# Optimization experiments

Hardware: AMD Instinct MI355X
Metric: run time of the kernel (lower is better)

The kernel has to match this reference:

```python
import jax, jax.numpy as jnp
import numpy as np

N, E, D0, D1, H = 20000, 640000, 64, 32, 64


def setup_inputs() -> dict:
    key = jax.random.key(0)
    ks = jax.random.split(key, 16)
    s = 0.1
    return {
        'feat0e': jax.random.normal(ks[0], (N, D0), jnp.float32),
        'feat1o': jax.random.normal(ks[1], (N, D1, 3), jnp.float32),
        'edge_attr': jax.random.normal(ks[2], (E, H), jnp.float32),
        'pos': jax.random.normal(ks[3], (N, 3), jnp.float32),
        'edge_index': jax.random.randint(ks[4], (2, E), 0, N, jnp.int64),
        # edge_net: FullyConnectedNet([H]*3 -> [H]) with silu
        'W1': jax.random.normal(ks[5], (H, H), jnp.float32) * s,
        'b1': jnp.zeros((H,), jnp.float32),
        'W2': jax.random.normal(ks[6], (H, H), jnp.float32) * s,
        'b2': jnp.zeros((H,), jnp.float32),
        'W3': jax.random.normal(ks[7], (H, H), jnp.float32) * s,
        'b3': jnp.zeros((H,), jnp.float32),
        # tensor-product path weights (internal weights, not shared)
        'w_ss': jax.random.normal(ks[8], (D0, H, D0), jnp.float32) * s,     # 0e x 0e -> 0e
        'w_vv': jax.random.normal(ks[9], (D1, D0), jnp.float32) * s,        # 1o . 1o -> 0e
        'w_sv': jax.random.normal(ks[10], (D0, D1), jnp.float32) * s,       # 0e x 1o -> 1o
        'w_vs': jax.random.normal(ks[11], (D1, H, D1), jnp.float32) * s,    # 1o x 0e -> 1o
        'w_cross': jax.random.normal(ks[12], (D1, D1), jnp.float32) * s,    # 1o x 1o -> 1o (cross)
        # gate: scalars -> per-vector-channel gates
        'Wg': jax.random.normal(ks[13], (D0, D1), jnp.float32) * s,
        'bg': jnp.zeros((D1,), jnp.float32),
    }


def reference(feat0e, feat1o, edge_attr, pos, edge_index,
              W1, b1, W2, b2, W3, b3,
              w_ss, w_vv, w_sv, w_vs, w_cross, Wg, bg):
    src, dst = edge_index[0], edge_index[1]

    # edge MLP (silu)
    h = jax.nn.silu(edge_attr @ W1 + b1)
    h = jax.nn.silu(h @ W2 + b2)
    edge_scalar = h @ W3 + b3                      # [E, H]

    rel_pos = pos[dst] - pos[src]                  # [E, 3]
    s_src = feat0e[src]                            # [E, D0]
    v_src = feat1o[src]                            # [E, D1, 3]

    # equivariant tensor product per edge
    dot_vv = jnp.sum(v_src * rel_pos[:, None, :], axis=-1)          # [E, D1]
    msg0e = (jnp.einsum('ep,eh,pho->eo', s_src, edge_scalar, w_ss)
             + dot_vv @ w_vv)                                        # [E, D0]
    cross_vv = jnp.cross(v_src, rel_pos[:, None, :])                 # [E, D1, 3]
    msg1o = (jnp.einsum('ep,pc,ex->ecx', s_src, w_sv, rel_pos)
             + jnp.einsum('edx,eh,dhc->ecx', v_src, edge_scalar, w_vs)
             + jnp.einsum('edx,dc->ecx', cross_vv, w_cross))          # [E, D1, 3]

    # scatter_mean over destination nodes
    counts = jax.ops.segment_sum(jnp.ones((E,), msg0e.dtype), dst, num_segments=N)
    denom = jnp.maximum(counts, 1.0)
    aggr0e = jax.ops.segment_sum(msg0e, dst, num_segments=N) / denom[:, None]
    aggr1o = jax.ops.segment_sum(msg1o, dst, num_segments=N) / denom[:, None, None]

    # gate + residual
    out0e = jax.nn.silu(aggr0e) + feat0e                              # [N, D0]
    gates = jax.nn.silu(aggr0e @ Wg + bg)                             # [N, D1]
    out1o = aggr1o * gates[:, :, None] + feat1o                       # [N, D1, 3]

    # concat flattened outputs into one array [N, D0 + 3*D1]
    return jnp.concatenate([out0e, out1o.reshape(N, D1 * 3)], axis=-1)
```

## Files before the change

kernel.cpp:

```cpp
#include <hip/hip_runtime.h>


#define NN 20000
#define EE 640000
#define EPMAX 940032

typedef _Float16 half8 __attribute__((ext_vector_type(8)));
typedef float f32x4 __attribute__((ext_vector_type(4)));

__device__ __forceinline__ float silu_f(float x) { return x / (1.0f + __expf(-x)); }
__device__ __forceinline__ _Float16 u2h(unsigned short u) {
    union { unsigned short u; _Float16 h; } c; c.u = u; return c.h;
}
__device__ __forceinline__ unsigned short h2u(_Float16 h) {
    union { unsigned short u; _Float16 h; } c; c.h = h; return c.u;
}
__device__ __forceinline__ half8 pack8(float4 a, float4 b) {
    half8 h;
    h[0]=(_Float16)a.x; h[1]=(_Float16)a.y; h[2]=(_Float16)a.z; h[3]=(_Float16)a.w;
    h[4]=(_Float16)b.x; h[5]=(_Float16)b.y; h[6]=(_Float16)b.z; h[7]=(_Float16)b.w;
    return h;
}

#define OFF_HIST  0ull
#define OFF_RS    81920ull
#define OFF_CUR   163840ull
#define OFF_FLAG  245760ull
#define F_OUTD    262144ull
#define F_PSP     360448ull
#define F_CURS    458752ull
#define F_POSOF   557056ull
#define F_AUX     3117056ull
#define F_DSTP    23597056ull
#define F_PDP     27357184ull
#define F_WMLP    31117312ull
#define F_WSV     31141888ull
#define F_WX2     31145984ull
#define F_WVV     31148032ull
#define F_WSSG    31152128ull
#define F_WVS3    31676416ull
#define F_ES      31807488ull
#define F_MSG0    152131584ull
#define F_MSG1    234051584ull
#define F_GH      356931584ull
#define NEED_F(npp) (F_GH + (unsigned long long)(npp) * 20480ull)

__global__ void detect_idx_kernel(const int* __restrict__ eidx, int* __restrict__ flag) {
    int odd_nz = 0, even_nz = 0;
    for (int k = 0; k < 64; ++k) {
        if (eidx[2 * k + 1] != 0) odd_nz = 1;
        if (eidx[2 * k] != 0) even_nz = 1;
    }
    *flag = (!odd_nz && even_nz) ? 1 : 0;
}

__device__ __forceinline__ void load_sd(const int* eidx, const int* flag, int e,
                                        int& s_, int& d_) {
    if (*flag) { s_ = (int)((const long long*)eidx)[e]; d_ = (int)((const long long*)eidx)[EE + e]; }
    else       { s_ = eidx[e];                          d_ = eidx[EE + e]; }
}

__global__ __launch_bounds__(256) void hist2_kernel(
    const int* __restrict__ eidx, const int* __restrict__ flag,
    int* __restrict__ hist, int* __restrict__ outd)
{
    const int e = blockIdx.x * 256 + threadIdx.x;
    int s_, d_; load_sd(eidx, flag, e, s_, d_);
    atomicAdd(hist + d_, 1);
    atomicAdd(outd + s_, 1);
}

__global__ __launch_bounds__(1024) void scan_kernel(
    const int* __restrict__ hist, int* __restrict__ rs, int* __restrict__ cur)
{
    __shared__ int part[1024];
    const int t = threadIdx.x;
    const int base = t * 20;
    int loc[20];
    int tot = 0;
#pragma unroll
    for (int k = 0; k < 20; ++k) {
        int n = base + k;
        int h = (n < NN) ? hist[n] : 0;
        loc[k] = tot; tot += h;
    }
    part[t] = tot;
    __syncthreads();
    for (int off = 1; off < 1024; off <<= 1) {
        int v = (t >= off) ? part[t - off] : 0;
        __syncthreads();
        part[t] += v;
        __syncthreads();
    }
    int excl = part[t] - tot;
#pragma unroll
    for (int k = 0; k < 20; ++k) {
        int n = base + k;
        if (n < NN) { rs[n] = excl + loc[k]; cur[n] = excl + loc[k]; }
    }
    if (t == 1023) rs[NN] = part[1023];
}

__global__ __launch_bounds__(1024) void scanP_kernel(
    const int* __restrict__ outd, int* __restrict__ psP, int* __restrict__ curS)
{
    __shared__ int part[1024];
    const int t = threadIdx.x;
    const int base = t * 20;
    int loc[20];
    int tot = 0;
#pragma unroll
    for (int k = 0; k < 20; ++k) {
        int n = base + k;
        int p = (n < NN) ? ((outd[n] + 15) & ~15) : 0;
        loc[k] = tot; tot += p;
    }
    part[t] = tot;
    __syncthreads();
    for (int off = 1; off < 1024; off <<= 1) {
        int v = (t >= off) ? part[t - off] : 0;
        __syncthreads();
        part[t] += v;
        __syncthreads();
    }
    int excl = part[t] - tot;
#pragma unroll
    for (int k = 0; k < 20; ++k) {
        int n = base + k;
        if (n < NN) { psP[n] = excl + loc[k]; curS[n] = excl + loc[k]; }
    }
}

__global__ __launch_bounds__(256) void scat_src_kernel(
    const int* __restrict__ eidx, const int* __restrict__ flag,
    int* __restrict__ curS, int* __restrict__ cur,
    int* __restrict__ dstP, int* __restrict__ pdP, int* __restrict__ posof)
{
    const int e = blockIdx.x * 256 + threadIdx.x;
    int s_, d_; load_sd(eidx, flag, e, s_, d_);
    int posS = atomicAdd(curS + s_, 1);
    int posD = atomicAdd(cur + d_, 1);
    dstP[posS] = d_; pdP[posS] = posD; posof[e] = posS;
}

__global__ __launch_bounds__(256) void prep2_kernel(
    const float* __restrict__ wss, const float* __restrict__ wvv,
    const float* __restrict__ wsv, const float* __restrict__ wvs,
    const float* __restrict__ wx,
    const float* __restrict__ W1, const float* __restrict__ W2,
    const float* __restrict__ W3, char* __restrict__ ws)
{
    int id = blockIdx.x * 256 + threadIdx.x;
    if (id >= 43136) return;
    int l = id & 63;
    int l4 = l >> 4, l16 = l & 15;
    half8 o;
    _Float16* dst;
    if (id < 32768) {
        int i = id;
        int f = i >> 6;
        int q = f >> 3, kfp = (f >> 2) & 1, nfp = f & 3;
#pragma unroll
        for (int j = 0; j < 8; j++) {
            int p = kfp * 32 + l4 * 8 + j;
            int cc = q * 64 + nfp * 16 + l16;
            int jc = cc & 7, lc = (cc >> 3) & 63, fi = cc >> 9;
            int kfc = fi >> 2, nfc = fi & 3;
            int h = kfc * 32 + (lc >> 4) * 8 + jc;
            int oo = nfc * 16 + (lc & 15);
            o[j] = (_Float16)wss[((size_t)p * 64 + h) * 64 + oo];
        }
        dst = (_Float16*)(ws + F_WSSG) + (size_t)i * 8;
    } else if (id < 40960) {
        int i = id - 32768;
        int f = i >> 6;
        int col = f * 16 + l16;
#pragma unroll
        for (int j = 0; j < 8; j++) {
            int d = l4 * 8 + j;
            o[j] = (_Float16)wvs[((size_t)d * 64 + (col & 63)) * 32 + (col >> 6)];
        }
        dst = (_Float16*)(ws + F_WVS3) + (size_t)i * 8;
    } else if (id < 42496) {
        int i = id - 40960; int f = i >> 6;
        int layer = f >> 3, kf = (f >> 2) & 1, nf = f & 3;
        const float* W = layer == 0 ? W1 : (layer == 1 ? W2 : W3);
#pragma unroll
        for (int j = 0; j < 8; j++)
            o[j] = (_Float16)W[(kf * 32 + l4 * 8 + j) * 64 + nf * 16 + l16];
        dst = (_Float16*)(ws + F_WMLP) + (size_t)i * 8;
    } else if (id < 42752) {
        int i = id - 42496; int nf = i >> 6;
#pragma unroll
        for (int j = 0; j < 8; j++)
            o[j] = (_Float16)wvv[(l4 * 8 + j) * 64 + nf * 16 + l16];
        dst = (_Float16*)(ws + F_WVV) + (size_t)i * 8;
    } else if (id < 43008) {
        int i = id - 42752; int frag = i >> 6;
        int kf = frag >> 1, nf = frag & 1;
#pragma unroll
        for (int j = 0; j < 8; j++)
            o[j] = (_Float16)wsv[(kf * 32 + l4 * 8 + j) * 32 + nf * 16 + l16];
        dst = (_Float16*)(ws + F_WSV) + (size_t)i * 8;
    } else {
        int i = id - 43008; int nf = i >> 6;
#pragma unroll
        for (int j = 0; j < 8; j++)
            o[j] = (_Float16)wx[(l4 * 8 + j) * 32 + nf * 16 + l16];
        dst = (_Float16*)(ws + F_WX2) + (size_t)i * 8;
    }
    *(half8*)dst = o;
}

__global__ __launch_bounds__(256, 4) void gG2_kernel(
    const float* __restrict__ feat0e, const char* __restrict__ wsp,
    int lo, int hi, _Float16* __restrict__ GH, _Float16* __restrict__ aux)
{
    const int tid = threadIdx.x, w = tid >> 6, lane = tid & 63;
    const int l4 = lane >> 4, l16 = lane & 15;
    const int n0 = lo + blockIdx.x * 16;
    if (n0 >= hi) return;

    half8 af[2];
    {
        int n = n0 + l16; if (n >= NN) n = NN - 1;
        const float* sp = feat0e + (size_t)n * 64 + l4 * 8;
        af[0] = pack8(*(const float4*)sp, *(const float4*)(sp + 4));
        af[1] = pack8(*(const float4*)(sp + 32), *(const float4*)(sp + 36));
    }
    const half8* wg = (const half8*)(wsp + F_WSSG);
#pragma unroll 2
    for (int qq = 0; qq < 16; ++qq) {
        const int q = w * 16 + qq;
        f32x4 acc[4];
#pragma unroll
        for (int nf = 0; nf < 4; nf++) acc[nf] = (f32x4){0.f,0.f,0.f,0.f};
#pragma unroll
        for (int kf = 0; kf < 2; kf++)
#pragma unroll
            for (int nf = 0; nf < 4; nf++)
                acc[nf] = __builtin_amdgcn_mfma_f32_16x16x32_f16(
                    af[kf], wg[(q * 8 + kf * 4 + nf) * 64 + lane], acc[nf], 0, 0, 0);
#pragma unroll
        for (int nf = 0; nf < 4; nf++)
#pragma unroll
            for (int reg = 0; reg < 4; reg++) {
                int n = n0 + l4 * 4 + reg;
                if (n < hi && n < NN)
                    GH[(size_t)(n - lo) * 10240 + q * 64 + nf * 16 + l16] =
                        (_Float16)acc[nf][reg];
            }
    }
    if (w == 0) {
        const half8* wsvp = (const half8*)(wsp + F_WSV);
        f32x4 accg[2];
#pragma unroll
        for (int nf = 0; nf < 2; nf++) accg[nf] = (f32x4){0.f,0.f,0.f,0.f};
#pragma unroll
        for (int kf = 0; kf < 2; kf++)
#pragma unroll
            for (int nf = 0; nf < 2; nf++)
                accg[nf] = __builtin_amdgcn_mfma_f32_16x16x32_f16(
                    af[kf], wsvp[(kf * 2 + nf) * 64 + lane], accg[nf], 0, 0, 0);
#pragma unroll
        for (int nf = 0; nf < 2; nf++)
#pragma unroll
            for (int reg = 0; reg < 4; reg++) {
                int n = n0 + l4 * 4 + reg;
                if (n < hi && n < NN)
                    aux[(size_t)n * 512 + nf * 16 + l16] = (_Float16)accg[nf][reg];
            }
    }
}

__global__ __launch_bounds__(256, 4) void gH_kernel(
    const float* __restrict__ feat1o, const char* __restrict__ wsp,
    int lo, int hi, _Float16* __restrict__ GH, _Float16* __restrict__ aux)
{
    const int tid = threadIdx.x, w = tid >> 6, lane = tid & 63;
    const int l4 = lane >> 4, l16 = lane & 15;
    const int n0 = lo + blockIdx.x * 16;
    const int x = blockIdx.y;
    if (n0 >= hi) return;

    half8 av;
    {
        int nn = n0 + l16; if (nn >= NN) nn = NN - 1;
#pragma unroll
        for (int j = 0; j < 8; j++)
            av[j] = (_Float16)feat1o[(size_t)nn * 96 + (l4 * 8 + j) * 3 + x];
    }
    const half8* wvs3 = (const half8*)(wsp + F_WVS3);

#pragma unroll 4
    for (int ff = 0; ff < 32; ++ff) {
        const int f = w * 32 + ff;
        f32x4 acc = __builtin_amdgcn_mfma_f32_16x16x32_f16(
            av, wvs3[f * 64 + lane], (f32x4){0.f,0.f,0.f,0.f}, 0, 0, 0);
#pragma unroll
        for (int reg = 0; reg < 4; reg++) {
            int n = n0 + l4 * 4 + reg;
            if (n < hi && n < NN)
                GH[(size_t)(n - lo) * 10240 + 4096 + x * 2048 + f * 16 + l16] =
                    (_Float16)acc[reg];
        }
    }
    if (w == 0) {
        const half8* wvvp = (const half8*)(wsp + F_WVV);
        const half8* wx2  = (const half8*)(wsp + F_WX2);
#pragma unroll
        for (int nf = 0; nf < 4; ++nf) {
            f32x4 acc = __builtin_amdgcn_mfma_f32_16x16x32_f16(
                av, wvvp[nf * 64 + lane], (f32x4){0.f,0.f,0.f,0.f}, 0, 0, 0);
#pragma unroll
            for (int reg = 0; reg < 4; reg++) {
                int n = n0 + l4 * 4 + reg;
                if (n < hi && n < NN)
                    aux[(size_t)n * 512 + 128 + x * 64 + nf * 16 + l16] =
                        (_Float16)acc[reg];
            }
        }
#pragma unroll
        for (int nf = 0; nf < 2; ++nf) {
            f32x4 acc = __builtin_amdgcn_mfma_f32_16x16x32_f16(
                av, wx2[nf * 64 + lane], (f32x4){0.f,0.f,0.f,0.f}, 0, 0, 0);
#pragma unroll
            for (int reg = 0; reg < 4; reg++) {
                int n = n0 + l4 * 4 + reg;
                if (n < hi && n < NN)
                    aux[(size_t)n * 512 + 32 + x * 32 + nf * 16 + l16] =
                        (_Float16)acc[reg];
            }
        }
    }
}

__global__ __launch_bounds__(256, 2) void es_kernel(
    const float* __restrict__ edge_attr,
    const float* __restrict__ b1, const float* __restrict__ b2,
    const float* __restrict__ b3,
    const char* __restrict__ wsp, const int* __restrict__ posof,
    _Float16* __restrict__ es)
{
    __shared__ half8 wml[1536];
    __shared__ __align__(16) unsigned short xch[4][1024];

    const int tid = threadIdx.x, w = tid >> 6, lane = tid & 63;
    const int l4 = lane >> 4, l16 = lane & 15;

    {
        const half8* wm = (const half8*)(wsp + F_WMLP);
        for (int f = tid; f < 1536; f += 256) wml[f] = wm[f];
    }
    __syncthreads();

    const int e0 = blockIdx.x * 64 + w * 16;

    float bias[3][4];
#pragma unroll
    for (int nf = 0; nf < 4; nf++) {
        bias[0][nf] = b1[nf * 16 + l16];
        bias[1][nf] = b2[nf * 16 + l16];
        bias[2][nf] = b3[nf * 16 + l16];
    }

    half8 af[2];
    {
        const float* ap = edge_attr + (size_t)(e0 + l16) * 64 + l4 * 8;
        af[0] = pack8(*(const float4*)ap, *(const float4*)(ap + 4));
        af[1] = pack8(*(const float4*)(ap + 32), *(const float4*)(ap + 36));
    }

    unsigned short* x = xch[w];
    const int sw16 = (l16 & 7) << 3;

#pragma unroll
    for (int layer = 0; layer < 3; ++layer) {
        f32x4 acc[4];
#pragma unroll
        for (int nf = 0; nf < 4; nf++) acc[nf] = (f32x4){0.f,0.f,0.f,0.f};
#pragma unroll
        for (int kf = 0; kf < 2; kf++)
#pragma unroll
            for (int nf = 0; nf < 4; nf++)
                acc[nf] = __builtin_amdgcn_mfma_f32_16x16x32_f16(
                    af[kf], wml[(layer * 8 + kf * 4 + nf) * 64 + lane],
                    acc[nf], 0, 0, 0);
#pragma unroll
        for (int nf = 0; nf < 4; nf++)
#pragma unroll
            for (int reg = 0; reg < 4; reg++) {
                int row = l4 * 4 + reg;
                int col = nf * 16 + l16;
                float v = acc[nf][reg] + bias[layer][nf];
                if (layer < 2) v = silu_f(v);
                x[row * 64 + (col ^ ((row & 7) << 3))] = h2u((_Float16)v);
            }
        if (layer < 2) {
#pragma unroll
            for (int kf = 0; kf < 2; kf++)
                af[kf] = *(const half8*)&x[l16 * 64 + ((kf * 32 + l4 * 8) ^ sw16)];
        }
    }
#pragma unroll
    for (int i = 0; i < 2; i++) {
        int row16 = i * 8 + (lane >> 3);
        int ps = posof[e0 + row16];
        int c8 = lane & 7;
        half8 v = *(const half8*)&x[row16 * 64 + ((c8 * 8) ^ ((row16 & 7) << 3))];
        *(half8*)(es + (size_t)ps * 64 + c8 * 8) = v;
    }
}

__global__ __launch_bounds__(256, 3) void msg01_node_kernel(
    const float* __restrict__ pos,
    const char* __restrict__ wsp,
    const _Float16* __restrict__ GH,
    const _Float16* __restrict__ es,
    int lo, int hi,
    _Float16* __restrict__ msg0, _Float16* __restrict__ msg1)
{
    __shared__ __align__(16) unsigned short xch[4][16 * 104];
    __shared__ float relb[4][16][4];
    __shared__ unsigned short auxl[4][320];

    const int tid = threadIdx.x, w = tid >> 6, lane = tid & 63;
    const int l4 = lane >> 4, l16 = lane & 15;

    const int n = lo + blockIdx.x * 4 + w;
    if (n >= hi) return;
    const int deg = ((const int*)(wsp + F_OUTD))[n];
    if (deg == 0) return;
    const int base = ((const int*)(wsp + F_PSP))[n];
    const int* dstP = (const int*)(wsp + F_DSTP);
    const int* pdP  = (const int*)(wsp + F_PDP);

    const float pn0 = pos[n * 3 + 0], pn1 = pos[n * 3 + 1], pn2 = pos[n * 3 + 2];

    const size_t kbase = (size_t)(n - lo) * 10240;
    half8 Gr[8];
    {
        const half8* gn = (const half8*)(GH + kbase);
#pragma unroll
        for (int f = 0; f < 8; f++) Gr[f] = gn[f * 64 + lane];
    }
    half8 Hf[2][6];
    {
        const _Float16* Hg = GH + kbase + 4096;
#pragma unroll
        for (int x = 0; x < 3; x++)
#pragma unroll
            for (int nfc = 0; nfc < 2; nfc++)
#pragma unroll
                for (int kf = 0; kf < 2; kf++)
                    Hf[kf][x * 2 + nfc] = *(const half8*)(
                        Hg + x * 2048 + (nfc * 16 + l16) * 64 + kf * 32 + l4 * 8);
    }
    {
        const _Float16* ag = (const _Float16*)(wsp + F_AUX) + (size_t)n * 512;
        for (int i = lane; i < 320; i += 64) auxl[w][i] = h2u(ag[i]);
    }

    unsigned short* x = xch[w];
    const int ntile = (deg + 15) >> 4;

    for (int t = 0; t < ntile; ++t) {
        const int r0 = t * 16;
        int rowc = r0 + l16; if (rowc > deg - 1) rowc = deg - 1;
        const int dd = dstP[base + rowc];
        const float rel0 = pos[dd * 3 + 0] - pn0;
        const float rel1 = pos[dd * 3 + 1] - pn1;
        const float rel2 = pos[dd * 3 + 2] - pn2;
        if (l4 == 0) {
            relb[w][l16][0] = rel0; relb[w][l16][1] = rel1; relb[w][l16][2] = rel2;
        }

        half8 esf[2];
        {
            const _Float16* ep = es + (size_t)(base + rowc) * 64;
            esf[0] = *(const half8*)(ep + l4 * 8);
            esf[1] = *(const half8*)(ep + 32 + l4 * 8);
        }

        {
            f32x4 acc0[4];
#pragma unroll
            for (int nf = 0; nf < 4; nf++) acc0[nf] = (f32x4){0.f,0.f,0.f,0.f};
#pragma unroll
            for (int kf = 0; kf < 2; kf++)
#pragma unroll
                for (int nf = 0; nf < 4; nf++)
                    acc0[nf] = __builtin_amdgcn_mfma_f32_16x16x32_f16(
                        esf[kf], Gr[kf * 4 + nf], acc0[nf], 0, 0, 0);
#pragma unroll
            for (int nf = 0; nf < 4; nf++) {
                float vw0 = (float)u2h(auxl[w][128 + 0 * 64 + nf * 16 + l16]);
                float vw1 = (float)u2h(auxl[w][128 + 1 * 64 + nf * 16 + l16]);
                float vw2 = (float)u2h(auxl[w][128 + 2 * 64 + nf * 16 + l16]);
#pragma unroll
                for (int reg = 0; reg < 4; reg++) {
                    int row = l4 * 4 + reg;
                    float v = acc0[nf][reg]
                            + relb[w][row][0] * vw0
                            + relb[w][row][1] * vw1
                            + relb[w][row][2] * vw2;
                    int col = nf * 16 + l16;
                    x[row * 104 + (col ^ ((row & 7) << 3))] = h2u((_Float16)v);
                }
            }
#pragma unroll
            for (int i = 0; i < 2; i++) {
                int row16 = i * 8 + (lane >> 3);
                if (r0 + row16 < deg) {
                    int rowD = pdP[base + r0 + row16];
                    int c8 = lane & 7;
                    half8 v = *(const half8*)&x[row16 * 104 + ((c8 * 8) ^ ((row16 & 7) << 3))];
                    *(half8*)(msg0 + (size_t)rowD * 64 + c8 * 8) = v;
                }
            }
        }

        {
            f32x4 acc1[6];
#pragma unroll
            for (int nf = 0; nf < 6; nf++) acc1[nf] = (f32x4){0.f,0.f,0.f,0.f};
#pragma unroll
            for (int kf = 0; kf < 2; kf++)
#pragma unroll
                for (int nf = 0; nf < 6; nf++)
                    acc1[nf] = __builtin_amdgcn_mfma_f32_16x16x32_f16(
                        esf[kf], Hf[kf][nf], acc1[nf], 0, 0, 0);
#pragma unroll
            for (int nf = 0; nf < 6; nf++) {
                const int xx = nf >> 1;
                const int x1 = (xx + 1) % 3, x2 = (xx + 2) % 3;
                const int c = (nf & 1) * 16 + l16;
                const float gv  = (float)u2h(auxl[w][c]);
                const float cw1 = (float)u2h(auxl[w][32 + x1 * 32 + c]);
                const float cw2 = (float)u2h(auxl[w][32 + x2 * 32 + c]);
#pragma unroll
                for (int reg = 0; reg < 4; reg++) {
                    int row = l4 * 4 + reg;
                    float val = acc1[nf][reg]
                              + gv * relb[w][row][xx]
                              + relb[w][row][x2] * cw1
                              - relb[w][row][x1] * cw2;
                    int col = nf * 16 + l16;
                    x[row * 104 + (col ^ ((row & 3) << 3))] = h2u((_Float16)val);
                }
            }
            const int rowS = lane >> 2;
            if (r0 + rowS < deg) {
                int rowD = pdP[base + r0 + rowS];
                const int swr = (rowS & 3) << 3;
#pragma unroll
                for (int t3 = 0; t3 < 3; t3++) {
                    int co = ((lane & 3) + 4 * t3) * 8;
                    half8 v = *(const half8*)&x[rowS * 104 + (co ^ swr)];
                    *(half8*)(msg1 + (size_t)rowD * 96 + co) = v;
                }
            }
        }
    }
}

__global__ __launch_bounds__(256) void gather0_kernel(
    const float* __restrict__ feat0e,
    const float* __restrict__ Wg, const float* __restrict__ bg,
    const char* __restrict__ wsp, const _Float16* __restrict__ msg0,
    float* __restrict__ out)
{
    __shared__ float Wgl[2048];
    __shared__ float ag[4][64];
    const int tid = threadIdx.x, w = tid >> 6, lane = tid & 63;
    for (int t = tid; t < 2048; t += 256) Wgl[t] = Wg[t];

    const int n = blockIdx.x * 4 + w;
    const int* rs = (const int*)(wsp + OFF_RS);
    const int i0 = rs[n], i1 = rs[n + 1];
    const int r8 = lane >> 3, c8 = lane & 7;

    float a[8];
#pragma unroll
    for (int j = 0; j < 8; j++) a[j] = 0.f;
    for (int i = i0 + r8; i < i1; i += 8) {
        half8 m = *(const half8*)(msg0 + (size_t)i * 64 + c8 * 8);
#pragma unroll
        for (int j = 0; j < 8; j++) a[j] += (float)m[j];
    }
#pragma unroll
    for (int s = 8; s < 64; s <<= 1)
#pragma unroll
        for (int j = 0; j < 8; j++) a[j] += __shfl_xor(a[j], s);
    if (r8 == 0)
#pragma unroll
        for (int j = 0; j < 8; j++) ag[w][c8 * 8 + j] = a[j];
    __syncthreads();

    const float inv = 1.0f / fmaxf((float)(i1 - i0), 1.0f);
    float av = ag[w][lane] * inv;
    out[(size_t)n * 160 + lane] = silu_f(av) + feat0e[(size_t)n * 64 + lane];

    if (lane < 32) {
        float gs = bg[lane];
#pragma unroll
        for (int p = 0; p < 64; ++p) gs = fmaf(ag[w][p] * inv, Wgl[p * 32 + lane], gs);
        out[(size_t)n * 160 + 64 + lane] = silu_f(gs);
    }
}

__global__ __launch_bounds__(256) void gather1_kernel(
    const float* __restrict__ feat1o,
    const char* __restrict__ wsp, const _Float16* __restrict__ msg1,
    float* __restrict__ out)
{
    __shared__ float ag1[4][96];
    __shared__ float gl[4][32];
    const int tid = threadIdx.x, w = tid >> 6, lane = tid & 63;
    const int n = blockIdx.x * 4 + w;
    const int* rs = (const int*)(wsp + OFF_RS);
    const int i0 = rs[n], i1 = rs[n + 1];

    if (lane < 32) gl[w][lane] = out[(size_t)n * 160 + 64 + lane];

    const int r4 = lane >> 4, c12 = lane & 15;
    float a[8];
#pragma unroll
    for (int j = 0; j < 8; j++) a[j] = 0.f;
    if (c12 < 12)
        for (int i = i0 + r4; i < i1; i += 4) {
            half8 m = *(const half8*)(msg1 + (size_t)i * 96 + c12 * 8);
#pragma unroll
            for (int j = 0; j < 8; j++) a[j] += (float)m[j];
        }
#pragma unroll
    for (int s = 16; s < 64; s <<= 1)
#pragma unroll
        for (int j = 0; j < 8; j++) a[j] += __shfl_xor(a[j], s);
    if (r4 == 0 && c12 < 12)
#pragma unroll
        for (int j = 0; j < 8; j++) ag1[w][c12 * 8 + j] = a[j];
    __syncthreads();

    const float inv = 1.0f / fmaxf((float)(i1 - i0), 1.0f);
#pragma unroll
    for (int t = 0; t < 2; t++) {
        int idx = t * 64 + lane;
        if (idx < 96) {
            int c = idx / 3, xx = idx - 3 * c;
            float v = ag1[w][xx * 32 + c] * inv * gl[w][c] + feat1o[(size_t)n * 96 + idx];
            out[(size_t)n * 160 + 64 + idx] = v;
        }
    }
}

extern "C" void kernel_launch(void* const* d_in, const int* in_sizes, int n_in,
                              void* d_out, int out_size, void* d_ws, size_t ws_size,
                              hipStream_t stream) {
    const float* feat0e    = (const float*)d_in[0];
    const float* feat1o    = (const float*)d_in[1];
    const float* edge_attr = (const float*)d_in[2];
    const float* pos       = (const float*)d_in[3];
    const int*   eidx      = (const int*)d_in[4];
    const float* W1 = (const float*)d_in[5];
    const float* b1 = (const float*)d_in[6];
    const float* W2 = (const float*)d_in[7];
    const float* b2 = (const float*)d_in[8];
    const float* W3 = (const float*)d_in[9];
    const float* b3 = (const float*)d_in[10];
    const float* wss    = (const float*)d_in[11];
    const float* wvv    = (const float*)d_in[12];
    const float* wsv    = (const float*)d_in[13];
    const float* wvs    = (const float*)d_in[14];
    const float* wcross = (const float*)d_in[15];
    const float* Wg = (const float*)d_in[16];
    const float* bg = (const float*)d_in[17];

    float* out = (float*)d_out;
    char*  ws  = (char*)d_ws;
    int* hist = (int*)(ws + OFF_HIST);
    int* rs   = (int*)(ws + OFF_RS);
    int* cur  = (int*)(ws + OFF_CUR);
    int* flag = (int*)(ws + OFF_FLAG);
    int* outd = (int*)(ws + F_OUTD);
    int* psP  = (int*)(ws + F_PSP);
    int* curS = (int*)(ws + F_CURS);
    int* posof= (int*)(ws + F_POSOF);
    int* dstP = (int*)(ws + F_DSTP);
    int* pdP  = (int*)(ws + F_PDP);
    _Float16* aux   = (_Float16*)(ws + F_AUX);
    _Float16* esb   = (_Float16*)(ws + F_ES);
    _Float16* msg0F = (_Float16*)(ws + F_MSG0);
    _Float16* msg1F = (_Float16*)(ws + F_MSG1);
    _Float16* GH    = (_Float16*)(ws + F_GH);

    int nppF = 0;
    const int cands[6] = {20000, 10000, 5000, 2500, 1250, 625};
    for (int i = 0; i < 6; ++i)
        if (ws_size >= NEED_F(cands[i])) { nppF = cands[i]; break; }
    if (nppF == 0) return;

    detect_idx_kernel<<<1, 1, 0, stream>>>(eidx, flag);
    hipMemsetAsync(ws + OFF_HIST, 0, NN * sizeof(int), stream);
    hipMemsetAsync(ws + F_OUTD, 0, NN * sizeof(int), stream);

    hist2_kernel<<<EE / 256, 256, 0, stream>>>(eidx, flag, hist, outd);
    scan_kernel<<<1, 1024, 0, stream>>>(hist, rs, cur);
    scanP_kernel<<<1, 1024, 0, stream>>>(outd, psP, curS);
    scat_src_kernel<<<EE / 256, 256, 0, stream>>>(
        eidx, flag, curS, cur, dstP, pdP, posof);
    prep2_kernel<<<(43136 + 255) / 256, 256, 0, stream>>>(
        wss, wvv, wsv, wvs, wcross, W1, W2, W3, ws);

    es_kernel<<<EE / 64, 256, 0, stream>>>(
        edge_attr, b1, b2, b3, (const char*)ws, posof, esb);

    const int S = (NN + nppF - 1) / nppF;
    for (int s = 0; s < S; ++s) {
        int lo = s * nppF;
        int hi = lo + nppF; if (hi > NN) hi = NN;
        const int ngroups = (hi - lo + 15) / 16;
        gG2_kernel<<<ngroups, 256, 0, stream>>>(
            feat0e, (const char*)ws, lo, hi, GH, aux);
        gH_kernel<<<dim3(ngroups, 3), 256, 0, stream>>>(
            feat1o, (const char*)ws, lo, hi, GH, aux);
        msg01_node_kernel<<<(hi - lo + 3) / 4, 256, 0, stream>>>(
            pos, (const char*)ws, GH, esb, lo, hi, msg0F, msg1F);
    }
    gather0_kernel<<<NN / 4, 256, 0, stream>>>(
        feat0e, Wg, bg, (const char*)ws, msg0F, out);
    gather1_kernel<<<NN / 4, 256, 0, stream>>>(
        feat1o, (const char*)ws, msg1F, out);
}
```

Measured before the change: 819.7 us.

## Fuse setup, node-transform, and gather kernels; interleave message buffers

Merges the two scan kernels into one launch and folds the edge scatter (source/destination slot assignment) into the edge-MLP kernel, which removes the posof buffer. Combines the scalar and vector node-transform kernels into one grid using blockIdx.y, and writes msg0/msg1 into a single interleaved 160-wide buffer so one gather kernel can reduce both and compute gates without reading them back from the output. The message kernel also prefetches the first tile's destination index and edge-scalar values, and loads aux with vector loads. The main savings are fewer launches and fewer intermediate global round-trips. The cost is that the atomics now sit inside the MLP kernel, and the interleaved stride may change gather coalescing.

```diff
diff --git a/kernel.cpp b/kernel.cpp
--- a/kernel.cpp
+++ b/kernel.cpp
@@ -29,20 +29,18 @@
 #define F_OUTD    262144ull
 #define F_PSP     360448ull
 #define F_CURS    458752ull
-#define F_POSOF   557056ull
-#define F_AUX     3117056ull
-#define F_DSTP    23597056ull
-#define F_PDP     27357184ull
-#define F_WMLP    31117312ull
-#define F_WSV     31141888ull
-#define F_WX2     31145984ull
-#define F_WVV     31148032ull
-#define F_WSSG    31152128ull
-#define F_WVS3    31676416ull
-#define F_ES      31807488ull
-#define F_MSG0    152131584ull
-#define F_MSG1    234051584ull
-#define F_GH      356931584ull
+#define F_AUX     557056ull
+#define F_DSTP    21037056ull
+#define F_PDP     24797184ull
+#define F_WMLP    28557312ull
+#define F_WSV     28581888ull
+#define F_WX2     28585984ull
+#define F_WVV     28588032ull
+#define F_WSSG    28592128ull
+#define F_WVS3    29116416ull
+#define F_ES      29247488ull
+#define F_MSG     149571584ull
+#define F_GH      354371584ull
 #define NEED_F(npp) (F_GH + (unsigned long long)(npp) * 20480ull)
 
 __global__ void detect_idx_kernel(const int* __restrict__ eidx, int* __restrict__ flag) {
@@ -70,77 +68,62 @@
     atomicAdd(outd + s_, 1);
 }
 
-__global__ __launch_bounds__(1024) void scan_kernel(
-    const int* __restrict__ hist, int* __restrict__ rs, int* __restrict__ cur)
+__global__ __launch_bounds__(1024) void scan2_kernel(
+    const int* __restrict__ hist, const int* __restrict__ outd,
+    int* __restrict__ rs, int* __restrict__ cur,
+    int* __restrict__ psP, int* __restrict__ curS)
 {
     __shared__ int part[1024];
     const int t = threadIdx.x;
     const int base = t * 20;
-    int loc[20];
-    int tot = 0;
-#pragma unroll
-    for (int k = 0; k < 20; ++k) {
-        int n = base + k;
-        int h = (n < NN) ? hist[n] : 0;
-        loc[k] = tot; tot += h;
-    }
-    part[t] = tot;
+    {
+        int loc[20]; int tot = 0;
+#pragma unroll
+        for (int k = 0; k < 20; ++k) {
+            int n = base + k;
+            int h = (n < NN) ? hist[n] : 0;
+            loc[k] = tot; tot += h;
+        }
+        part[t] = tot;
+        __syncthreads();
+        for (int off = 1; off < 1024; off <<= 1) {
+            int v = (t >= off) ? part[t - off] : 0;
+            __syncthreads();
+            part[t] += v;
+            __syncthreads();
+        }
+        int excl = part[t] - tot;
+#pragma unroll
+        for (int k = 0; k < 20; ++k) {
+            int n = base + k;
+            if (n < NN) { rs[n] = excl + loc[k]; cur[n] = excl + loc[k]; }
+        }
+        if (t == 1023) rs[NN] = part[1023];
+    }
     __syncthreads();
-    for (int off = 1; off < 1024; off <<= 1) {
-        int v = (t >= off) ? part[t - off] : 0;
+    {
+        int loc[20]; int tot = 0;
+#pragma unroll
+        for (int k = 0; k < 20; ++k) {
+            int n = base + k;
+            int p = (n < NN) ? ((outd[n] + 15) & ~15) : 0;
+            loc[k] = tot; tot += p;
+        }
+        part[t] = tot;
         __syncthreads();
-        part[t] += v;
-        __syncthreads();
-    }
-    int excl = part[t] - tot;
-#pragma unroll
-    for (int k = 0; k < 20; ++k) {
-        int n = base + k;
-        if (n < NN) { rs[n] = excl + loc[k]; cur[n] = excl + loc[k]; }
-    }
-    if (t == 1023) rs[NN] = part[1023];
-}
-
-__global__ __launch_bounds__(1024) void scanP_kernel(
-    const int* __restrict__ outd, int* __restrict__ psP, int* __restrict__ curS)
-{
-    __shared__ int part[1024];
-    const int t = threadIdx.x;
-    const int base = t * 20;
-    int loc[20];
-    int tot = 0;
-#pragma unroll
-    for (int k = 0; k < 20; ++k) {
-        int n = base + k;
-        int p = (n < NN) ? ((outd[n] + 15) & ~15) : 0;
-        loc[k] = tot; tot += p;
-    }
-    part[t] = tot;
-    __syncthreads();
-    for (int off = 1; off < 1024; off <<= 1) {
-        int v = (t >= off) ? part[t - off] : 0;
-        __syncthreads();
-        part[t] += v;
-        __syncthreads();
-    }
-    int excl = part[t] - tot;
-#pragma unroll
-    for (int k = 0; k < 20; ++k) {
-        int n = base + k;
-        if (n < NN) { psP[n] = excl + loc[k]; curS[n] = excl + loc[k]; }
-    }
-}
-
-__global__ __launch_bounds__(256) void scat_src_kernel(
-    const int* __restrict__ eidx, const int* __restrict__ flag,
-    int* __restrict__ curS, int* __restrict__ cur,
-    int* __restrict__ dstP, int* __restrict__ pdP, int* __restrict__ posof)
-{
-    const int e = blockIdx.x * 256 + threadIdx.x;
-    int s_, d_; load_sd(eidx, flag, e, s_, d_);
-    int posS = atomicAdd(curS + s_, 1);
-    int posD = atomicAdd(cur + d_, 1);
-    dstP[posS] = d_; pdP[posS] = posD; posof[e] = posS;
+        for (int off = 1; off < 1024; off <<= 1) {
+            int v = (t >= off) ? part[t - off] : 0;
+            __syncthreads();
+            part[t] += v;
+            __syncthreads();
+        }
+        int excl = part[t] - tot;
+#pragma unroll
+        for (int k = 0; k < 20; ++k) {
+            int n = base + k;
+            if (n < NN) { psP[n] = excl + loc[k]; curS[n] = excl + loc[k]; }
+        }
+    }
 }
 
 __global__ __launch_bounds__(256) void prep2_kernel(
@@ -212,8 +195,9 @@
     *(half8*)dst = o;
 }
 
-__global__ __launch_bounds__(256, 4) void gG2_kernel(
-    const float* __restrict__ feat0e, const char* __restrict__ wsp,
+__global__ __launch_bounds__(256, 4) void gGH_kernel(
+    const float* __restrict__ feat0e, const float* __restrict__ feat1o,
+    const char* __restrict__ wsp,
     int lo, int hi, _Float16* __restrict__ GH, _Float16* __restrict__ aux)
 {
     const int tid = threadIdx.x, w = tid >> 6, lane = tid & 63;
@@ -221,115 +205,106 @@
     const int n0 = lo + blockIdx.x * 16;
     if (n0 >= hi) return;
 
-    half8 af[2];
-    {
-        int n = n0 + l16; if (n >= NN) n = NN - 1;
-        const float* sp = feat0e + (size_t)n * 64 + l4 * 8;
-        af[0] = pack8(*(const float4*)sp, *(const float4*)(sp + 4));
-        af[1] = pack8(*(const float4*)(sp + 32), *(const float4*)(sp + 36));
-    }
-    const half8* wg = (const half8*)(wsp + F_WSSG);
+    if (blockIdx.y == 0) {
+        half8 af[2];
+        {
+            int n = n0 + l16; if (n >= NN) n = NN - 1;
+            const float* sp = feat0e + (size_t)n * 64 + l4 * 8;
+            af[0] = pack8(*(const float4*)sp, *(const float4*)(sp + 4));
+            af[1] = pack8(*(const float4*)(sp + 32), *(const float4*)(sp + 36));
+        }
+        const half8* wg = (const half8*)(wsp + F_WSSG);
 #pragma unroll 2
-    for (int qq = 0; qq < 16; ++qq) {
-        const int q = w * 16 + qq;
-        f32x4 acc[4];
-#pragma unroll
-        for (int nf = 0; nf < 4; nf++) acc[nf] = (f32x4){0.f,0.f,0.f,0.f};
-#pragma unroll
-        for (int kf = 0; kf < 2; kf++)
+        for (int qq = 0; qq < 16; ++qq) {
+            const int q = w * 16 + qq;
+            f32x4 acc[4];
+#pragma unroll
+            for (int nf = 0; nf < 4; nf++) acc[nf] = (f32x4){0.f,0.f,0.f,0.f};
+#pragma unroll
+            for (int kf = 0; kf < 2; kf++)
+#pragma unroll
+                for (int nf = 0; nf < 4; nf++)
+                    acc[nf] = __builtin_amdgcn_mfma_f32_16x16x32_f16(
+                        af[kf], wg[(q * 8 + kf * 4 + nf) * 64 + lane], acc[nf], 0, 0, 0);
 #pragma unroll
             for (int nf = 0; nf < 4; nf++)
-                acc[nf] = __builtin_amdgcn_mfma_f32_16x16x32_f16(
-                    af[kf], wg[(q * 8 + kf * 4 + nf) * 64 + lane], acc[nf], 0, 0, 0);
-#pragma unroll
-        for (int nf = 0; nf < 4; nf++)
+#pragma unroll
+                for (int reg = 0; reg < 4; reg++) {
+                    int n = n0 + l4 * 4 + reg;
+                    if (n < hi && n < NN)
+                        GH[(size_t)(n - lo) * 10240 + q * 64 + nf * 16 + l16] =
+                            (_Float16)acc[nf][reg];
+                }
+        }
+        if (w == 0) {
+            const half8* wsvp = (const half8*)(wsp + F_WSV);
+            f32x4 accg[2];
+#pragma unroll
+            for (int nf = 0; nf < 2; nf++) accg[nf] = (f32x4){0.f,0.f,0.f,0.f};
+#pragma unroll
+            for (int kf = 0; kf < 2; kf++)
+#pragma unroll
+                for (int nf = 0; nf < 2; nf++)
+                    accg[nf] = __builtin_amdgcn_mfma_f32_16x16x32_f16(
+                        af[kf], wsvp[(kf * 2 + nf) * 64 + lane], accg[nf], 0, 0, 0);
+#pragma unroll
+            for (int nf = 0; nf < 2; nf++)
+#pragma unroll
+                for (int reg = 0; reg < 4; reg++) {
+                    int n = n0 + l4 * 4 + reg;
+                    if (n < hi && n < NN)
+                        aux[(size_t)n * 512 + nf * 16 + l16] = (_Float16)accg[nf][reg];
+                }
+        }
+    } else {
+        const int x = blockIdx.y - 1;
+        half8 av;
+        {
+            int nn = n0 + l16; if (nn >= NN) nn = NN - 1;
+#pragma unroll
+            for (int j = 0; j < 8; j++)
+                av[j] = (_Float16)feat1o[(size_t)nn * 96 + (l4 * 8 + j) * 3 + x];
+        }
+        const half8* wvs3 = (const half8*)(wsp + F_WVS3);
+#pragma unroll 4
+        for (int ff = 0; ff < 32; ++ff) {
+            const int f = w * 32 + ff;
+            f32x4 acc = __builtin_amdgcn_mfma_f32_16x16x32_f16(
+                av, wvs3[f * 64 + lane], (f32x4){0.f,0.f,0.f,0.f}, 0, 0, 0);
 #pragma unroll
             for (int reg = 0; reg < 4; reg++) {
                 int n = n0 + l4 * 4 + reg;
                 if (n < hi && n < NN)
-                    GH[(size_t)(n - lo) * 10240 + q * 64 + nf * 16 + l16] =
-                        (_Float16)acc[nf][reg];
-            }
-    }
-    if (w == 0) {
-        const half8* wsvp = (const half8*)(wsp + F_WSV);
-        f32x4 accg[2];
-#pragma unroll
-        for (int nf = 0; nf < 2; nf++) accg[nf] = (f32x4){0.f,0.f,0.f,0.f};
-#pragma unroll
-        for (int kf = 0; kf < 2; kf++)
-#pragma unroll
-            for (int nf = 0; nf < 2; nf++)
-                accg[nf] = __builtin_amdgcn_mfma_f32_16x16x32_f16(
-                    af[kf], wsvp[(kf * 2 + nf) * 64 + lane], accg[nf], 0, 0, 0);
-#pragma unroll
-        for (int nf = 0; nf < 2; nf++)
-#pragma unroll
-            for (int reg = 0; reg < 4; reg++) {
-                int n = n0 + l4 * 4 + reg;
-                if (n < hi && n < NN)
-                    aux[(size_t)n * 512 + nf * 16 + l16] = (_Float16)accg[nf][reg];
-            }
-    }
-}
-
-__global__ __launch_bounds__(256, 4) void gH_kernel(
-    const float* __restrict__ feat1o, const char* __restrict__ wsp,
-    int lo, int hi, _Float16* __restrict__ GH, _Float16* __restrict__ aux)
-{
-    const int tid = threadIdx.x, w = tid >> 6, lane = tid & 63;
-    const int l4 = lane >> 4, l16 = lane & 15;
-    const int n0 = lo + blockIdx.x * 16;
-    const int x = blockIdx.y;
-    if (n0 >= hi) return;
-
-    half8 av;
-    {
-        int nn = n0 + l16; if (nn >= NN) nn = NN - 1;
-#pragma unroll
-        for (int j = 0; j < 8; j++)
-            av[j] = (_Float16)feat1o[(size_t)nn * 96 + (l4 * 8 + j) * 3 + x];
-    }
-    const half8* wvs3 = (const half8*)(wsp + F_WVS3);
-
-#pragma unroll 4
-    for (int ff = 0; ff < 32; ++ff) {
-        const int f = w * 32 + ff;
-        f32x4 acc = __builtin_amdgcn_mfma_f32_16x16x32_f16(
-            av, wvs3[f * 64 + lane], (f32x4){0.f,0.f,0.f,0.f}, 0, 0, 0);
-#pragma unroll
-        for (int reg = 0; reg < 4; reg++) {
-            int n = n0 + l4 * 4 + reg;
-            if (n < hi && n < NN)
-                GH[(size_t)(n - lo) * 10240 + 4096 + x * 2048 + f * 16 + l16] =
-                    (_Float16)acc[reg];
-        }
-    }
-    if (w == 0) {
-        const half8* wvvp = (const half8*)(wsp + F_WVV);
-        const half8* wx2  = (const half8*)(wsp + F_WX2);
-#pragma unroll
-        for (int nf = 0; nf < 4; ++nf) {
-            f32x4 acc = __builtin_amdgcn_mfma_f32_16x16x32_f16(
-                av, wvvp[nf * 64 + lane], (f32x4){0.f,0.f,0.f,0.f}, 0, 0, 0);
-#pragma unroll
-            for (int reg = 0; reg < 4; reg++) {
-                int n = n0 + l4 * 4 + reg;
-                if (n < hi && n < NN)
-                    aux[(size_t)n * 512 + 128 + x * 64 + nf * 16 + l16] =
+                    GH[(size_t)(n - lo) * 10240 + 4096 + x * 2048 + f * 16 + l16] =
                         (_Float16)acc[reg];
             }
         }
-#pragma unroll
-        for (int nf = 0; nf < 2; ++nf) {
-            f32x4 acc = __builtin_amdgcn_mfma_f32_16x16x32_f16(
-                av, wx2[nf * 64 + lane], (f32x4){0.f,0.f,0.f,0.f}, 0, 0, 0);
-#pragma unroll
-            for (int reg = 0; reg < 4; reg++) {
-                int n = n0 + l4 * 4 + reg;
-                if (n < hi && n < NN)
-                    aux[(size_t)n * 512 + 32 + x * 32 + nf * 16 + l16] =
-                        (_Float16)acc[reg];
+        if (w == 0) {
+            const half8* wvvp = (const half8*)(wsp + F_WVV);
+            const half8* wx2  = (const half8*)(wsp + F_WX2);
+#pragma unroll
+            for (int nf = 0; nf < 4; ++nf) {
+                f32x4 acc = __builtin_amdgcn_mfma_f32_16x16x32_f16(
+                    av, wvvp[nf * 64 + lane], (f32x4){0.f,0.f,0.f,0.f}, 0, 0, 0);
+#pragma unroll
+                for (int reg = 0; reg < 4; reg++) {
+                    int n = n0 + l4 * 4 + reg;
+                    if (n < hi && n < NN)
+                        aux[(size_t)n * 512 + 128 + x * 64 + nf * 16 + l16] =
+                            (_Float16)acc[reg];
+                }
+            }
+#pragma unroll
+            for (int nf = 0; nf < 2; ++nf) {
+                f32x4 acc = __builtin_amdgcn_mfma_f32_16x16x32_f16(
+                    av, wx2[nf * 64 + lane], (f32x4){0.f,0.f,0.f,0.f}, 0, 0, 0);
+#pragma unroll
+                for (int reg = 0; reg < 4; reg++) {
+                    int n = n0 + l4 * 4 + reg;
+                    if (n < hi && n < NN)
+                        aux[(size_t)n * 512 + 32 + x * 32 + nf * 16 + l16] =
+                            (_Float16)acc[reg];
+                }
             }
         }
     }
@@ -339,22 +314,33 @@
     const float* __restrict__ edge_attr,
     const float* __restrict__ b1, const float* __restrict__ b2,
     const float* __restrict__ b3,
-    const char* __restrict__ wsp, const int* __restrict__ posof,
+    const char* __restrict__ wsp,
+    const int* __restrict__ eidx, const int* __restrict__ flag,
+    int* __restrict__ curS, int* __restrict__ cur,
+    int* __restrict__ dstP, int* __restrict__ pdP,
     _Float16* __restrict__ es)
 {
     __shared__ half8 wml[1536];
     __shared__ __align__(16) unsigned short xch[4][1024];
+    __shared__ int posl[4][16];
 
     const int tid = threadIdx.x, w = tid >> 6, lane = tid & 63;
     const int l4 = lane >> 4, l16 = lane & 15;
-
+    const int e0 = blockIdx.x * 64 + w * 16;
+
+    if (l4 == 0) {
+        int e = e0 + l16;
+        int s_, d_; load_sd(eidx, flag, e, s_, d_);
+        int posS = atomicAdd(curS + s_, 1);
+        int posD = atomicAdd(cur + d_, 1);
+        dstP[posS] = d_; pdP[posS] = posD;
+        posl[w][l16] = posS;
+    }
     {
         const half8* wm = (const half8*)(wsp + F_WMLP);
         for (int f = tid; f < 1536; f += 256) wml[f] = wm[f];
     }
     __syncthreads();
-
-    const int e0 = blockIdx.x * 64 + w * 16;
 
     float bias[3][4];
 #pragma unroll
@@ -405,7 +391,7 @@
 #pragma unroll
     for (int i = 0; i < 2; i++) {
         int row16 = i * 8 + (lane >> 3);
-        int ps = posof[e0 + row16];
+        int ps = posl[w][row16];
         int c8 = lane & 7;
         half8 v = *(const half8*)&x[row16 * 64 + ((c8 * 8) ^ ((row16 & 7) << 3))];
         *(half8*)(es + (size_t)ps * 64 + c8 * 8) = v;
@@ -418,11 +404,11 @@
     const _Float16* __restrict__ GH,
     const _Float16* __restrict__ es,
     int lo, int hi,
-    _Float16* __restrict__ msg0, _Float16* __restrict__ msg1)
+    _Float16* __restrict__ msg)
 {
     __shared__ __align__(16) unsigned short xch[4][16 * 104];
     __shared__ float relb[4][16][4];
-    __shared__ unsigned short auxl[4][320];
+    __shared__ __align__(16) unsigned short auxl[4][320];
 
     const int tid = threadIdx.x, w = tid >> 6, lane = tid & 63;
     const int l4 = lane >> 4, l16 = lane & 15;
@@ -434,6 +420,16 @@
     const int base = ((const int*)(wsp + F_PSP))[n];
     const int* dstP = (const int*)(wsp + F_DSTP);
     const int* pdP  = (const int*)(wsp + F_PDP);
+    const int ntile = (deg + 15) >> 4;
+
+    int rowcA = l16 < deg - 1 ? l16 : deg - 1;
+    int ddA = dstP[base + rowcA];
+    half8 eA0, eA1;
+    {
+        const _Float16* ep = es + (size_t)(base + rowcA) * 64;
+        eA0 = *(const half8*)(ep + l4 * 8);
+        eA1 = *(const half8*)(ep + 32 + l4 * 8);
+    }
 
     const float pn0 = pos[n * 3 + 0], pn1 = pos[n * 3 + 1], pn2 = pos[n * 3 + 2];
 
@@ -458,28 +454,29 @@
     }
     {
         const _Float16* ag = (const _Float16*)(wsp + F_AUX) + (size_t)n * 512;
-        for (int i = lane; i < 320; i += 64) auxl[w][i] = h2u(ag[i]);
+        if (lane < 40) ((half8*)auxl[w])[lane] = ((const half8*)ag)[lane];
     }
 
     unsigned short* x = xch[w];
-    const int ntile = (deg + 15) >> 4;
 
     for (int t = 0; t < ntile; ++t) {
-        const int r0 = t * 16;
-        int rowc = r0 + l16; if (rowc > deg - 1) rowc = deg - 1;
-        const int dd = dstP[base + rowc];
-        const float rel0 = pos[dd * 3 + 0] - pn0;
-        const float rel1 = pos[dd * 3 + 1] - pn1;
-        const float rel2 = pos[dd * 3 + 2] - pn2;
+        const float rel0 = pos[ddA * 3 + 0] - pn0;
+        const float rel1 = pos[ddA * 3 + 1] - pn1;
+        const float rel2 = pos[ddA * 3 + 2] - pn2;
         if (l4 == 0) {
             relb[w][l16][0] = rel0; relb[w][l16][1] = rel1; relb[w][l16][2] = rel2;
         }
 
-        half8 esf[2];
-        {
-            const _Float16* ep = es + (size_t)(base + rowc) * 64;
-            esf[0] = *(const half8*)(ep + l4 * 8);
-            esf[1] = *(const half8*)(ep + 32 + l4 * 8);
+        half8 e0 = eA0, e1 = eA1;
+        const int r0 = t * 16;
+
+        if (t + 1 < ntile) {
+            int rc = (t + 1) * 16 + l16; if (rc > deg - 1) rc = deg - 1;
+            rowcA = rc;
+            ddA = dstP[base + rc];
+            const _Float16* ep = es + (size_t)(base + rc) * 64;
+            eA0 = *(const half8*)(ep + l4 * 8);
+            eA1 = *(const half8*)(ep + 32 + l4 * 8);
         }
 
         {
@@ -491,7 +488,7 @@
 #pragma unroll
                 for (int nf = 0; nf < 4; nf++)
                     acc0[nf] = __builtin_amdgcn_mfma_f32_16x16x32_f16(
-                        esf[kf], Gr[kf * 4 + nf], acc0[nf], 0, 0, 0);
+                        kf == 0 ? e0 : e1, Gr[kf * 4 + nf], acc0[nf], 0, 0, 0);
 #pragma unroll
             for (int nf = 0; nf < 4; nf++) {
                 float vw0 = (float)u2h(auxl[w][128 + 0 * 64 + nf * 16 + l16]);
@@ -515,7 +512,7 @@
                     int rowD = pdP[base + r0 + row16];
                     int c8 = lane & 7;
                     half8 v = *(const half8*)&x[row16 * 104 + ((c8 * 8) ^ ((row16 & 7) << 3))];
-                    *(half8*)(msg0 + (size_t)rowD * 64 + c8 * 8) = v;
+                    *(half8*)(msg + (size_t)rowD * 160 + c8 * 8) = v;
                 }
             }
         }
@@ -529,7 +526,7 @@
 #pragma unroll
                 for (int nf = 0; nf < 6; nf++)
                     acc1[nf] = __builtin_amdgcn_mfma_f32_16x16x32_f16(
-                        esf[kf], Hf[kf][nf], acc1[nf], 0, 0, 0);
+                        kf == 0 ? e0 : e1, Hf[kf][nf], acc1[nf], 0, 0, 0);
 #pragma unroll
             for (int nf = 0; nf < 6; nf++) {
                 const int xx = nf >> 1;
@@ -557,98 +554,83 @@
                 for (int t3 = 0; t3 < 3; t3++) {
                     int co = ((lane & 3) + 4 * t3) * 8;
                     half8 v = *(const half8*)&x[rowS * 104 + (co ^ swr)];
-                    *(half8*)(msg1 + (size_t)rowD * 96 + co) = v;
+                    *(half8*)(msg + (size_t)rowD * 160 + 64 + co) = v;
                 }
             }
         }
     }
 }
 
-__global__ __launch_bounds__(256) void gather0_kernel(
-    const float* __restrict__ feat0e,
+__global__ __launch_bounds__(256) void gather_kernel(
+    const float* __restrict__ feat0e, const float* __restrict__ feat1o,
     const float* __restrict__ Wg, const float* __restrict__ bg,
-    const char* __restrict__ wsp, const _Float16* __restrict__ msg0,
+    const char* __restrict__ wsp, const _Float16* __restrict__ msg,
     float* __restrict__ out)
 {
     __shared__ float Wgl[2048];
     __shared__ float ag[4][64];
+    __shared__ float ag1[4][96];
+    __shared__ float gate_lds[4][32];
     const int tid = threadIdx.x, w = tid >> 6, lane = tid & 63;
     for (int t = tid; t < 2048; t += 256) Wgl[t] = Wg[t];
+    __syncthreads();
 
     const int n = blockIdx.x * 4 + w;
     const int* rs = (const int*)(wsp + OFF_RS);
     const int i0 = rs[n], i1 = rs[n + 1];
-    const int r8 = lane >> 3, c8 = lane & 7;
-
-    float a[8];
-#pragma unroll
-    for (int j = 0; j < 8; j++) a[j] = 0.f;
-    for (int i = i0 + r8; i < i1; i += 8) {
-        half8 m = *(const half8*)(msg0 + (size_t)i * 64 + c8 * 8);
-#pragma unroll
-        for (int j = 0; j < 8; j++) a[j] += (float)m[j];
-    }
-#pragma unroll
-    for (int s = 8; s < 64; s <<= 1)
-#pragma unroll
-        for (int j = 0; j < 8; j++) a[j] += __shfl_xor(a[j], s);
-    if (r8 == 0)
-#pragma unroll
-        for (int j = 0; j < 8; j++) ag[w][c8 * 8 + j] = a[j];
-    __syncthreads();
+
+    {
+        const int r8 = lane >> 3, c8 = lane & 7;
+        float a[8];
+#pragma unroll
+        for (int j = 0; j < 8; j++) a[j] = 0.f;
+        for (int i = i0 + r8; i < i1; i += 8) {
+            half8 m = *(const half8*)(msg + (size_t)i * 160 + c8 * 8);
+#pragma unroll
+            for (int j = 0; j < 8; j++) a[j] += (float)m[j];
+        }
+#pragma unroll
+        for (int s = 8; s < 64; s <<= 1)
+#pragma unroll
+            for (int j = 0; j < 8; j++) a[j] += __shfl_xor(a[j], s);
+        if (r8 == 0)
+#pragma unroll
+            for (int j = 0; j < 8; j++) ag[w][c8 * 8 + j] = a[j];
+    }
+    {
+        const int r4 = lane >> 4, c12 = lane & 15;
+        float a[8];
+#pragma unroll
+        for (int j = 0; j < 8; j++) a[j] = 0.f;
+        if (c12 < 12)
+            for (int i = i0 + r4; i < i1; i += 4) {
+                half8 m = *(const half8*)(msg + (size_t)i * 160 + 64 + c12 * 8);
+#pragma unroll
+                for (int j = 0; j < 8; j++) a[j] += (float)m[j];
+            }
+#pragma unroll
+        for (int s = 16; s < 64; s <<= 1)
+#pragma unroll
+            for (int j = 0; j < 8; j++) a[j] += __shfl_xor(a[j], s);
+        if (r4 == 0 && c12 < 12)
+#pragma unroll
+            for (int j = 0; j < 8; j++) ag1[w][c12 * 8 + j] = a[j];
+    }
 
     const float inv = 1.0f / fmaxf((float)(i1 - i0), 1.0f);
-    float av = ag[w][lane] * inv;
-    out[(size_t)n * 160 + lane] = silu_f(av) + feat0e[(size_t)n * 64 + lane];
-
+    out[(size_t)n * 160 + lane] = silu_f(ag[w][lane] * inv) + feat0e[(size_t)n * 64 + lane];
     if (lane < 32) {
         float gs = bg[lane];
 #pragma unroll
         for (int p = 0; p < 64; ++p) gs = fmaf(ag[w][p] * inv, Wgl[p * 32 + lane], gs);
-        out[(size_t)n * 160 + 64 + lane] = silu_f(gs);
-    }
-}
-
-__global__ __launch_bounds__(256) void gather1_kernel(
-    const float* __restrict__ feat1o,
-    const char* __restrict__ wsp, const _Float16* __restrict__ msg1,
-    float* __restrict__ out)
-{
-    __shared__ float ag1[4][96];
-    __shared__ float gl[4][32];
-    const int tid = threadIdx.x, w = tid >> 6, lane = tid & 63;
-    const int n = blockIdx.x * 4 + w;
-    const int* rs = (const int*)(wsp + OFF_RS);
-    const int i0 = rs[n], i1 = rs[n + 1];
-
-    if (lane < 32) gl[w][lane] = out[(size_t)n * 160 + 64 + lane];
-
-    const int r4 = lane >> 4, c12 = lane & 15;
-    float a[8];
-#pragma unroll
-    for (int j = 0; j < 8; j++) a[j] = 0.f;
-    if (c12 < 12)
-        for (int i = i0 + r4; i < i1; i += 4) {
-            half8 m = *(const half8*)(msg1 + (size_t)i * 96 + c12 * 8);
-#pragma unroll
-            for (int j = 0; j < 8; j++) a[j] += (float)m[j];
-        }
-#pragma unroll
-    for (int s = 16; s < 64; s <<= 1)
-#pragma unroll
-        for (int j = 0; j < 8; j++) a[j] += __shfl_xor(a[j], s);
-    if (r4 == 0 && c12 < 12)
-#pragma unroll
-        for (int j = 0; j < 8; j++) ag1[w][c12 * 8 + j] = a[j];
-    __syncthreads();
-
-    const float inv = 1.0f / fmaxf((float)(i1 - i0), 1.0f);
+        gate_lds[w][lane] = silu_f(gs);
+    }
 #pragma unroll
     for (int t = 0; t < 2; t++) {
         int idx = t * 64 + lane;
         if (idx < 96) {
             int c = idx / 3, xx = idx - 3 * c;
-            float v = ag1[w][xx * 32 + c] * inv * gl[w][c] + feat1o[(size_t)n * 96 + idx];
+            float v = ag1[w][xx * 32 + c] * inv * gate_lds[w][c] + feat1o[(size_t)n * 96 + idx];
             out[(size_t)n * 160 + 64 + idx] = v;
         }
     }
@@ -685,14 +667,12 @@
     int* outd = (int*)(ws + F_OUTD);
     int* psP  = (int*)(ws + F_PSP);
     int* curS = (int*)(ws + F_CURS);
-    int* posof= (int*)(ws + F_POSOF);
     int* dstP = (int*)(ws + F_DSTP);
     int* pdP  = (int*)(ws + F_PDP);
-    _Float16* aux   = (_Float16*)(ws + F_AUX);
-    _Float16* esb   = (_Float16*)(ws + F_ES);
-    _Float16* msg0F = (_Float16*)(ws + F_MSG0);
-    _Float16* msg1F = (_Float16*)(ws + F_MSG1);
-    _Float16* GH    = (_Float16*)(ws + F_GH);
+    _Float16* aux  = (_Float16*)(ws + F_AUX);
+    _Float16* esb  = (_Float16*)(ws + F_ES);
+    _Float16* msgF = (_Float16*)(ws + F_MSG);
+    _Float16* GH   = (_Float16*)(ws + F_GH);
 
     int nppF = 0;
     const int cands[6] = {20000, 10000, 5000, 2500, 1250, 625};
@@ -705,30 +685,24 @@
     hipMemsetAsync(ws + F_OUTD, 0, NN * sizeof(int), stream);
 
     hist2_kernel<<<EE / 256, 256, 0, stream>>>(eidx, flag, hist, outd);
-    scan_kernel<<<1, 1024, 0, stream>>>(hist, rs, cur);
-    scanP_kernel<<<1, 1024, 0, stream>>>(outd, psP, curS);
-    scat_src_kernel<<<EE / 256, 256, 0, stream>>>(
-        eidx, flag, curS, cur, dstP, pdP, posof);
+    scan2_kernel<<<1, 1024, 0, stream>>>(hist, outd, rs, cur, psP, curS);
     prep2_kernel<<<(43136 + 255) / 256, 256, 0, stream>>>(
         wss, wvv, wsv, wvs, wcross, W1, W2, W3, ws);
 
     es_kernel<<<EE / 64, 256, 0, stream>>>(
-        edge_attr, b1, b2, b3, (const char*)ws, posof, esb);
+        edge_attr, b1, b2, b3, (const char*)ws, eidx, flag, curS, cur,
+        dstP, pdP, esb);
 
     const int S = (NN + nppF - 1) / nppF;
     for (int s = 0; s < S; ++s) {
         int lo = s * nppF;
         int hi = lo + nppF; if (hi > NN) hi = NN;
         const int ngroups = (hi - lo + 15) / 16;
-        gG2_kernel<<<ngroups, 256, 0, stream>>>(
-            feat0e, (const char*)ws, lo, hi, GH, aux);
-        gH_kernel<<<dim3(ngroups, 3), 256, 0, stream>>>(
-            feat1o, (const char*)ws, lo, hi, GH, aux);
+        gGH_kernel<<<dim3(ngroups, 4), 256, 0, stream>>>(
+            feat0e, feat1o, (const char*)ws, lo, hi, GH, aux);
         msg01_node_kernel<<<(hi - lo + 3) / 4, 256, 0, stream>>>(
-            pos, (const char*)ws, GH, esb, lo, hi, msg0F, msg1F);
-    }
-    gather0_kernel<<<NN / 4, 256, 0, stream>>>(
-        feat0e, Wg, bg, (const char*)ws, msg0F, out);
-    gather1_kernel<<<NN / 4, 256, 0, stream>>>(
-        feat1o, (const char*)ws, msg1F, out);
-}
+            pos, (const char*)ws, GH, esb, lo, hi, msgF);
+    }
+    gather_kernel<<<NN / 4, 256, 0, stream>>>(
+        feat0e, feat1o, Wg, bg, (const char*)ws, msgF, out);
+}
```

After: 705.0 us. -14.0%, faster.
